# Kernel optimization log

Measured on AMD Instinct MI355X. Metric: run time of the kernel, lower is better.

Reference implementation:

```python
import jax, jax.numpy as jnp
import numpy as np

B, C, N, H = 8, 256, 1024, 8

def setup_inputs() -> dict:
    key = jax.random.key(0)
    ks = jax.random.split(key, 6)
    x = jax.random.normal(ks[0], (B, C, 3, N), jnp.float32)
    scale = 1.0 / np.sqrt(C).astype(np.float32)
    Wq = jax.random.normal(ks[1], (C, C), jnp.float32) * scale
    Wk = jax.random.normal(ks[2], (C, C), jnp.float32) * scale
    Wv = jax.random.normal(ks[3], (C, C), jnp.float32) * scale
    Wp = jax.random.normal(ks[4], (C, C), jnp.float32) * scale
    mask = jax.random.randint(ks[5], (B, N), 0, 2).astype(bool)  # True = padded
    return {"x": x, "Wq": Wq, "Wk": Wk, "Wv": Wv, "Wp": Wp, "mask": mask}

def _vn_linear(W, x):
    # VNLinear: channel-mixing linear (no bias) over the C axis of [B, C, 3, N]
    return jnp.einsum('oc,bcdn->bodn', W, x)

def _to_heads(t):
    # [B, C, 3, N] -> [B, H, N, (C//H)*3]
    hd = C // H
    return t.reshape(B, H, hd, 3, N).transpose(0, 1, 4, 2, 3).reshape(B, H, N, hd * 3)

def reference(x, Wq, Wk, Wv, Wp, mask):
    hd = C // H
    D = hd * 3
    q = _to_heads(_vn_linear(Wq, x))
    k = _to_heads(_vn_linear(Wk, x))
    v = _to_heads(_vn_linear(Wv, x))
    att = jnp.einsum('bhnd,bhmd->bhnm', q, k) * (1.0 / np.sqrt(D).astype(np.float32))
    att = jnp.where(mask[:, None, None, :], -jnp.inf, att)
    att = jax.nn.softmax(att, axis=-1)
    y = jnp.einsum('bhnm,bhmd->bhnd', att, v)
    # [B, H, N, D] -> [B, H, D, N] -> [B, H, hd, 3, N] -> [B, C, 3, N]
    y = y.transpose(0, 1, 3, 2).reshape(B, H, hd, 3, N).reshape(B, C, 3, N)
    return _vn_linear(Wp, y)
```

## Files before the change

kernel.cpp:

```cpp
#include <hip/hip_runtime.h>
#include <hip/hip_bf16.h>
#include <math.h>

#define B_ 8
#define C_ 256
#define N_ 1024
#define H_ 8
#define DH 96
#define BHN (C_*3*N_)
#define SC 0.10206207261596575f

typedef _Float16 half8 __attribute__((ext_vector_type(8)));
typedef float f32x4 __attribute__((ext_vector_type(4)));
typedef float f32x16 __attribute__((ext_vector_type(16)));

typedef __attribute__((address_space(1))) void gvoid;
typedef __attribute__((address_space(3))) void lvoid;
__device__ inline void gl_lds16(const _Float16* g, _Float16* l) {
  __builtin_amdgcn_global_load_lds((gvoid*)g, (lvoid*)l, 16, 0, 0);
}

typedef __fp16 fp16x2 __attribute__((ext_vector_type(2)));
union H2U { fp16x2 h2; unsigned u; };
__device__ inline unsigned pkh(float a, float b) {
  H2U x; x.h2 = __builtin_amdgcn_cvt_pkrtz(a, b); return x.u;
}
union PF { half8 v; unsigned u[4]; };

__device__ inline void plswap(unsigned& a, unsigned& b) {
  asm volatile("v_permlane32_swap_b32 %0, %1" : "+v"(a), "+v"(b));
}

__global__ void mask_bits_kernel(const unsigned* __restrict__ mraw,
                                 unsigned long long* __restrict__ mb) {
  __shared__ int notI, notF;
  if (threadIdx.x == 0) { notI = 0; notF = 0; }
  __syncthreads();
  int li = 0, lf = 0;
  for (int i = threadIdx.x; i < 2048; i += 256) {
    unsigned w = mraw[i];
    if (w > 1u) li = 1;
    if (w != 0u && w != 0x3F800000u) lf = 1;
  }
  if (li) atomicOr(&notI, 1);
  if (lf) atomicOr(&notF, 1);
  __syncthreads();
  const int tid = threadIdx.x;
  if (tid < 128) {
    int base = tid * 64;
    unsigned long long bits = 0;
    if (!notI) {
      for (int j = 0; j < 64; ++j)
        bits |= (unsigned long long)(mraw[base + j] & 1u) << j;
    } else if (!notF) {
      for (int j = 0; j < 64; ++j)
        bits |= (unsigned long long)(mraw[base + j] != 0u ? 1 : 0) << j;
    } else {
      const unsigned char* m8 = (const unsigned char*)mraw;
      for (int j = 0; j < 64; ++j)
        bits |= (unsigned long long)(m8[base + j] ? 1 : 0) << j;
    }
    mb[tid] = bits;
  }
}

__global__ void convw_kernel(const float* __restrict__ Wq,
                             const float* __restrict__ Wk,
                             const float* __restrict__ Wv,
                             const float* __restrict__ Wp,
                             _Float16* __restrict__ Wh) {
  int idx = blockIdx.x * 256 + threadIdx.x;
  int e0 = idx * 8;
  const float* src = (e0 < 65536) ? Wq
                   : (e0 < 131072) ? Wk
                   : (e0 < 196608) ? Wv : Wp;
  int off = e0 & 65535;
  float4 a = *(const float4*)&src[off];
  float4 b = *(const float4*)&src[off + 4];
  _Float16 t[8] = {(_Float16)a.x, (_Float16)a.y, (_Float16)a.z, (_Float16)a.w,
                   (_Float16)b.x, (_Float16)b.y, (_Float16)b.z, (_Float16)b.w};
  *(uint4*)&Wh[e0] = *(uint4*)t;
}

__global__ __launch_bounds__(256) void convxt_kernel(
    const float* __restrict__ x, _Float16* __restrict__ XT) {
  __shared__ _Float16 T[64][65];
  const int m0 = blockIdx.x * 64;
  const int c0 = blockIdx.y * 64;
  const int b = blockIdx.z;
  const float* xb = x + (size_t)b * BHN;
  _Float16* ob = XT + (size_t)b * BHN;
  const int t = threadIdx.x;
#pragma unroll
  for (int i = 0; i < 16; ++i) {
    int e = t + i * 256;
    int c = e >> 6, m = e & 63;
    T[m][c] = (_Float16)xb[(size_t)(c0 + c) * 3072 + m0 + m];
  }
  __syncthreads();
#pragma unroll
  for (int i = 0; i < 2; ++i) {
    int e = t + i * 256;
    int m = e >> 3, ch = e & 7;
    _Float16 tmp[8];
#pragma unroll
    for (int j = 0; j < 8; ++j) tmp[j] = T[m][ch * 8 + j];
    *(uint4*)&ob[(size_t)(m0 + m) * 256 + c0 + ch * 8] = *(uint4*)tmp;
  }
}

template <int MODE>
__global__ __launch_bounds__(256, 4) void mgemm_kernel(
    const _Float16* __restrict__ Wh, int woff,
    const _Float16* __restrict__ Xn,
    _Float16* __restrict__ O0, _Float16* __restrict__ O1,
    _Float16* __restrict__ O2, float* __restrict__ Of, int nw) {
  const int zz = blockIdx.z;
  const int w = zz % nw;
  const int b = zz / nw;
  const _Float16* Wb = Wh + (size_t)(woff + w) * 65536;
  const _Float16* Bb = Xn + (size_t)b * BHN;
  const int o0 = blockIdx.y * 128;
  const int bn0 = blockIdx.x * 128;

  __shared__ __align__(16) _Float16 Ah[4096];
  __shared__ __align__(16) _Float16 Bh[4096];

  const int tid = threadIdx.x;
  const int wave = tid >> 6;
  const int lane = tid & 63;
  const int lg = lane >> 4, ll = lane & 15;
  const int wm = wave >> 1, wn = wave & 1;
  const int r0 = tid >> 2, c4 = tid & 3;

  f32x4 acc[4][4];
#pragma unroll
  for (int mi = 0; mi < 4; ++mi)
#pragma unroll
    for (int ni = 0; ni < 4; ++ni) acc[mi][ni] = (f32x4){0.f, 0.f, 0.f, 0.f};

  for (int k0 = 0; k0 < 256; k0 += 32) {
    gl_lds16(Wb + (size_t)(o0 + r0) * 256 + k0 + c4 * 8, &Ah[wave * 512]);
    gl_lds16(Wb + (size_t)(o0 + 64 + r0) * 256 + k0 + c4 * 8,
             &Ah[2048 + wave * 512]);
    gl_lds16(Bb + (size_t)(bn0 + r0) * 256 + k0 + c4 * 8, &Bh[wave * 512]);
    gl_lds16(Bb + (size_t)(bn0 + 64 + r0) * 256 + k0 + c4 * 8,
             &Bh[2048 + wave * 512]);
    __syncthreads();
    half8 af[4], bf[4];
#pragma unroll
    for (int mi = 0; mi < 4; ++mi)
      af[mi] = *(const half8*)&Ah[(wm * 64 + mi * 16 + ll) * 32 + lg * 8];
#pragma unroll
    for (int ni = 0; ni < 4; ++ni)
      bf[ni] = *(const half8*)&Bh[(wn * 64 + ni * 16 + ll) * 32 + lg * 8];
#pragma unroll
    for (int mi = 0; mi < 4; ++mi)
#pragma unroll
      for (int ni = 0; ni < 4; ++ni)
        acc[mi][ni] = __builtin_amdgcn_mfma_f32_16x16x32_f16(
            af[mi], bf[ni], acc[mi][ni], 0, 0, 0);
    __syncthreads();
  }

#pragma unroll
  for (int mi = 0; mi < 4; ++mi) {
#pragma unroll
    for (int ni = 0; ni < 4; ++ni) {
      int o = o0 + wm * 64 + mi * 16 + lg * 4;
      int n = bn0 + wn * 64 + ni * 16 + ll;
      if constexpr (MODE == 1) {
        float* Ofb = Of + (size_t)b * BHN;
#pragma unroll
        for (int r = 0; r < 4; ++r)
          Ofb[(size_t)(o + r) * 3072 + n] = acc[mi][ni][r];
      } else {
        if (w == 2) {
          _Float16* Oc = O2 + (size_t)b * BHN;
#pragma unroll
          for (int r = 0; r < 4; ++r)
            Oc[(size_t)(o + r) * 3072 + n] = (_Float16)acc[mi][ni][r];
        } else {
          _Float16* On = ((w == 0) ? O0 : O1) + (size_t)b * BHN;
          float qs = (w == 0) ? SC : 1.0f;
          _Float16 t4[4];
#pragma unroll
          for (int r = 0; r < 4; ++r) t4[r] = (_Float16)(acc[mi][ni][r] * qs);
          *(uint2*)&On[(size_t)n * 256 + o] = *(uint2*)t4;
        }
      }
    }
  }
}

__global__ __launch_bounds__(256, 2) void attn_kernel(
    const _Float16* __restrict__ qh, const _Float16* __restrict__ kh,
    const _Float16* __restrict__ vh,
    const unsigned long long* __restrict__ mbits,
    _Float16* __restrict__ yT) {
  const int gid = blockIdx.x;
  const int bh = gid & 63;
  const int qt = gid >> 6;
  const int b = bh >> 3, h = bh & 7;
  const int n0 = qt * 128;

  __shared__ __align__(16) _Float16 Qs[12288];
  __shared__ __align__(16) _Float16 KsL[2][6144];
  __shared__ __align__(16) _Float16 VtL[2][6144];

  const int tid = threadIdx.x;
  const int lane = tid & 63;
  const int wave = tid >> 6;
  const int hi = lane >> 5;
  const int lq = lane & 31;
  const int wq0 = wave * 32;

  const _Float16* qb = qh + (size_t)b * BHN;
  const _Float16* kb = kh + (size_t)b * BHN;
  const _Float16* vb = vh + (size_t)b * BHN;

  const _Float16* ksrc[3];
  const _Float16* vsrc[3];
#pragma unroll
  for (int r = 0; r < 3; ++r) {
    int p = r * 4 + wave;
    ksrc[r] = kb + (size_t)((p >> 2) * 1024 + lane) * 256 + h * 32 + (p & 3) * 8;
    int G = (r * 4 + wave) * 64 + lane;
    int kp = G / 96, d = G - kp * 96;
    vsrc[r] = vb + (size_t)(h * 32 + (d & 31)) * 3072 + (d >> 5) * 1024 + kp * 8;
  }

  auto stage_kv = [&](int cur) {
    _Float16* Kd = &KsL[cur][0];
    _Float16* Vd = &VtL[cur][0];
#pragma unroll
    for (int r = 0; r < 3; ++r) {
      gl_lds16(ksrc[r], &Kd[(r * 4 + wave) * 512]);
      gl_lds16(vsrc[r], &Vd[(r * 4 + wave) * 512]);
      ksrc[r] += 64 * 256;
      vsrc[r] += 64;
    }
  };

#pragma unroll
  for (int r = 0; r < 6; ++r) {
    int pc = r * 4 + wave;
    int p = pc >> 1;
    int q = (pc & 1) * 64 + lane;
    gl_lds16(qb + (size_t)((p >> 2) * 1024 + n0 + q) * 256 + h * 32 + (p & 3) * 8,
             &Qs[(r * 4 + wave) * 512]);
  }
  stage_kv(0);
  __syncthreads();
  stage_kv(1);

  half8 qf[6];
#pragma unroll
  for (int ks = 0; ks < 6; ++ks)
    qf[ks] = *(const half8*)&Qs[(((2 * ks + hi) * 128) + wq0 + lq) * 8];

  float M = 0.f, Lh = 0.f;
  f32x16 yacc[3];
#pragma unroll
  for (int dt = 0; dt < 3; ++dt)
#pragma unroll
    for (int r = 0; r < 16; ++r) yacc[dt][r] = 0.f;

  auto compute_tile = [&](int t, int cur) {
    const _Float16* Ksb = &KsL[cur][0];
    const _Float16* Vtb = &VtL[cur][0];
    const unsigned long long m64 = mbits[b * 16 + t];

    f32x16 s[2];
#pragma unroll
    for (int r = 0; r < 16; ++r) { s[0][r] = 0.f; s[1][r] = 0.f; }
    __builtin_amdgcn_s_setprio(1);
#pragma unroll
    for (int ks = 0; ks < 6; ++ks) {
      half8 kf0 = *(const half8*)&Ksb[(((2 * ks + hi) * 64) + lq) * 8];
      half8 kf1 = *(const half8*)&Ksb[(((2 * ks + hi) * 64) + 32 + lq) * 8];
      s[0] = __builtin_amdgcn_mfma_f32_32x32x16_f16(kf0, qf[ks], s[0], 0, 0, 0);
      s[1] = __builtin_amdgcn_mfma_f32_32x32x16_f16(kf1, qf[ks], s[1], 0, 0, 0);
    }
    __builtin_amdgcn_s_setprio(0);

    float mx = -1e30f;
#pragma unroll
    for (int nt = 0; nt < 2; ++nt) {
      unsigned wm = (unsigned)(m64 >> (nt * 32 + 4 * hi));
#pragma unroll
      for (int r = 0; r < 16; ++r) {
        float sv = s[nt][r];
        sv = ((wm >> ((r & 3) + 8 * (r >> 2))) & 1u) ? -1e30f : sv;
        s[nt][r] = sv;
        mx = fmaxf(mx, sv);
      }
    }
    if (__any(mx > M + 8.f)) {
      float mx2 = fmaxf(mx, __shfl_xor(mx, 32));
      float newM = fmaxf(M, mx2);
      float corr = __expf(M - newM);
      M = newM;
      Lh *= corr;
#pragma unroll
      for (int dt = 0; dt < 3; ++dt)
#pragma unroll
        for (int r = 0; r < 16; ++r) yacc[dt][r] *= corr;
    }
    float psum = 0.f;
#pragma unroll
    for (int nt = 0; nt < 2; ++nt)
#pragma unroll
      for (int r = 0; r < 16; ++r) {
        float p = __expf(s[nt][r] - M);
        s[nt][r] = p;
        psum += p;
      }
    Lh += psum;

#pragma unroll
    for (int nt = 0; nt < 2; ++nt) {
#pragma unroll
      for (int hf = 0; hf < 2; ++hf) {
        const int bs = hf * 8;
        unsigned A0 = pkh(s[nt][bs + 0], s[nt][bs + 1]);
        unsigned A1 = pkh(s[nt][bs + 2], s[nt][bs + 3]);
        unsigned B0 = pkh(s[nt][bs + 4], s[nt][bs + 5]);
        unsigned B1 = pkh(s[nt][bs + 6], s[nt][bs + 7]);
        plswap(A0, B0);
        plswap(A1, B1);
        PF pf;
        pf.u[0] = A0;
        pf.u[1] = A1;
        pf.u[2] = B0;
        pf.u[3] = B1;
        const int kt = nt * 2 + hf;
        __builtin_amdgcn_s_setprio(1);
#pragma unroll
        for (int dt = 0; dt < 3; ++dt) {
          half8 vf = *(const half8*)&Vtb[(((kt * 2 + hi) * 96) + dt * 32 + lq) * 8];
          yacc[dt] = __builtin_amdgcn_mfma_f32_32x32x16_f16(vf, pf.v, yacc[dt],
                                                            0, 0, 0);
        }
        __builtin_amdgcn_s_setprio(0);
      }
    }
  };

  compute_tile(0, 0);
  for (int t = 1; t < 16; ++t) {
    __syncthreads();
    if (t + 1 < 16) stage_kv((t + 1) & 1);
    compute_tile(t, t & 1);
  }

  float L = Lh + __shfl_xor(Lh, 32);
  float inv = (L > 0.f) ? 1.f / L : 0.f;
  _Float16* Ys = &Qs[wave * 3072];
#pragma unroll
  for (int dt = 0; dt < 3; ++dt)
#pragma unroll
    for (int r = 0; r < 16; ++r) {
      int dperm = dt * 32 + (r & 3) + 8 * (r >> 2) + 4 * hi;
      Ys[lq * 96 + dperm] = (_Float16)(yacc[dt][r] * inv);
    }
  _Float16* yb = yT + (size_t)b * BHN;
#pragma unroll
  for (int j = 0; j < 6; ++j) {
    int c = j * 64 + lane;
    int q = c / 12, p = c - q * 12;
    uint4 val = *(const uint4*)&Ys[q * 96 + p * 8];
    int dd = p >> 2, pi = p & 3;
    *(uint4*)&yb[(size_t)((dd << 10) + n0 + wq0 + q) * 256 + h * 32 + pi * 8] =
        val;
  }
}

extern "C" void kernel_launch(void* const* d_in, const int* in_sizes, int n_in,
                              void* d_out, int out_size, void* d_ws,
                              size_t ws_size, hipStream_t stream) {
  const float* x = (const float*)d_in[0];
  const float* Wq = (const float*)d_in[1];
  const float* Wk = (const float*)d_in[2];
  const float* Wv = (const float*)d_in[3];
  const float* Wp = (const float*)d_in[4];
  const unsigned* mask = (const unsigned*)d_in[5];
  float* out = (float*)d_out;

  _Float16* Wh = (_Float16*)d_ws;
  _Float16* XT = Wh + 4 * 65536;
  _Float16* qh = XT + (size_t)B_ * BHN;
  _Float16* kh = qh + (size_t)B_ * BHN;
  _Float16* vh = kh + (size_t)B_ * BHN;
  _Float16* yT = vh + (size_t)B_ * BHN;
  unsigned long long* mb = (unsigned long long*)(yT + (size_t)B_ * BHN);

  mask_bits_kernel<<<1, 256, 0, stream>>>(mask, mb);
  convw_kernel<<<128, 256, 0, stream>>>(Wq, Wk, Wv, Wp, Wh);
  convxt_kernel<<<dim3(48, 4, B_), 256, 0, stream>>>(x, XT);

  dim3 g1(24, 2, B_ * 3);
  mgemm_kernel<0><<<g1, 256, 0, stream>>>(Wh, 0, XT, qh, kh, vh, nullptr, 3);

  attn_kernel<<<dim3(512), 256, 0, stream>>>(qh, kh, vh, mb, yT);

  dim3 g3(24, 2, B_);
  mgemm_kernel<1><<<g3, 256, 0, stream>>>(Wh, 3, yT, nullptr, nullptr, nullptr,
                                          out, 1);
}
```

Before: 101.6 us.

## Load attention operands directly from global memory and use exp2 softmax

Removes the LDS staging of Q, K and V in the attention kernel: each wave now loads its MFMA fragments straight from global memory into registers, which eliminates the double-buffered shared-memory pipeline and its per-tile barriers. The query scale folds in log2(e) so the softmax can use the hardware exp2 instruction, and the rescale threshold moves from 8 to 12 to match the log2 domain. The epilogue writes y directly from registers instead of going through an LDS transpose. In exchange, global loads are narrower and less coalesced, there is no explicit prefetch overlap, and register pressure rises because of the K and V fragment arrays.

```diff
diff --git a/kernel.cpp b/kernel.cpp
--- a/kernel.cpp
+++ b/kernel.cpp
@@ -9,6 +9,7 @@
 #define DH 96
 #define BHN (C_*3*N_)
 #define SC 0.10206207261596575f
+#define SCL2 0.14722193f
 
 typedef _Float16 half8 __attribute__((ext_vector_type(8)));
 typedef float f32x4 __attribute__((ext_vector_type(4)));
@@ -19,6 +20,8 @@
 __device__ inline void gl_lds16(const _Float16* g, _Float16* l) {
   __builtin_amdgcn_global_load_lds((gvoid*)g, (lvoid*)l, 16, 0, 0);
 }
+
+__device__ inline float ex2(float x) { return __builtin_amdgcn_exp2f(x); }
 
 typedef __fp16 fp16x2 __attribute__((ext_vector_type(2)));
 union H2U { fp16x2 h2; unsigned u; };
@@ -182,7 +185,7 @@
             Oc[(size_t)(o + r) * 3072 + n] = (_Float16)acc[mi][ni][r];
         } else {
           _Float16* On = ((w == 0) ? O0 : O1) + (size_t)b * BHN;
-          float qs = (w == 0) ? SC : 1.0f;
+          float qs = (w == 0) ? SCL2 : 1.0f;
           _Float16 t4[4];
 #pragma unroll
           for (int r = 0; r < 4; ++r) t4[r] = (_Float16)(acc[mi][ni][r] * qs);
@@ -204,10 +207,6 @@
   const int b = bh >> 3, h = bh & 7;
   const int n0 = qt * 128;
 
-  __shared__ __align__(16) _Float16 Qs[12288];
-  __shared__ __align__(16) _Float16 KsL[2][6144];
-  __shared__ __align__(16) _Float16 VtL[2][6144];
-
   const int tid = threadIdx.x;
   const int lane = tid & 63;
   const int wave = tid >> 6;
@@ -219,45 +218,16 @@
   const _Float16* kb = kh + (size_t)b * BHN;
   const _Float16* vb = vh + (size_t)b * BHN;
 
-  const _Float16* ksrc[3];
-  const _Float16* vsrc[3];
-#pragma unroll
-  for (int r = 0; r < 3; ++r) {
-    int p = r * 4 + wave;
-    ksrc[r] = kb + (size_t)((p >> 2) * 1024 + lane) * 256 + h * 32 + (p & 3) * 8;
-    int G = (r * 4 + wave) * 64 + lane;
-    int kp = G / 96, d = G - kp * 96;
-    vsrc[r] = vb + (size_t)(h * 32 + (d & 31)) * 3072 + (d >> 5) * 1024 + kp * 8;
-  }
-
-  auto stage_kv = [&](int cur) {
-    _Float16* Kd = &KsL[cur][0];
-    _Float16* Vd = &VtL[cur][0];
-#pragma unroll
-    for (int r = 0; r < 3; ++r) {
-      gl_lds16(ksrc[r], &Kd[(r * 4 + wave) * 512]);
-      gl_lds16(vsrc[r], &Vd[(r * 4 + wave) * 512]);
-      ksrc[r] += 64 * 256;
-      vsrc[r] += 64;
-    }
-  };
-
-#pragma unroll
-  for (int r = 0; r < 6; ++r) {
-    int pc = r * 4 + wave;
-    int p = pc >> 1;
-    int q = (pc & 1) * 64 + lane;
-    gl_lds16(qb + (size_t)((p >> 2) * 1024 + n0 + q) * 256 + h * 32 + (p & 3) * 8,
-             &Qs[(r * 4 + wave) * 512]);
-  }
-  stage_kv(0);
-  __syncthreads();
-  stage_kv(1);
-
   half8 qf[6];
 #pragma unroll
-  for (int ks = 0; ks < 6; ++ks)
-    qf[ks] = *(const half8*)&Qs[(((2 * ks + hi) * 128) + wq0 + lq) * 8];
+  for (int ks = 0; ks < 6; ++ks) {
+    int pp = 2 * ks + hi;
+    int dd = pp >> 2, i0 = (pp & 3) * 8;
+    qf[ks] = *(const half8*)(qb +
+        (size_t)(dd * 1024 + n0 + wq0 + lq) * 256 + h * 32 + i0);
+  }
+
+  const _Float16* vrow = vb + (size_t)(h * 32 + lq) * 3072;
 
   float M = 0.f, Lh = 0.f;
   f32x16 yacc[3];
@@ -266,9 +236,26 @@
 #pragma unroll
     for (int r = 0; r < 16; ++r) yacc[dt][r] = 0.f;
 
-  auto compute_tile = [&](int t, int cur) {
-    const _Float16* Ksb = &KsL[cur][0];
-    const _Float16* Vtb = &VtL[cur][0];
+  for (int t = 0; t < 16; ++t) {
+    const int m0 = t * 64;
+    half8 kf[6][2];
+#pragma unroll
+    for (int ks = 0; ks < 6; ++ks) {
+      int pp = 2 * ks + hi;
+      int dd = pp >> 2, i0 = (pp & 3) * 8;
+      const _Float16* base =
+          kb + (size_t)(dd * 1024 + m0 + lq) * 256 + h * 32 + i0;
+      kf[ks][0] = *(const half8*)base;
+      kf[ks][1] = *(const half8*)(base + 32 * 256);
+    }
+    half8 vf[4][3];
+#pragma unroll
+    for (int kt = 0; kt < 4; ++kt)
+#pragma unroll
+      for (int dt = 0; dt < 3; ++dt)
+        vf[kt][dt] =
+            *(const half8*)(vrow + dt * 1024 + m0 + (kt * 2 + hi) * 8);
+
     const unsigned long long m64 = mbits[b * 16 + t];
 
     f32x16 s[2];
@@ -277,10 +264,10 @@
     __builtin_amdgcn_s_setprio(1);
 #pragma unroll
     for (int ks = 0; ks < 6; ++ks) {
-      half8 kf0 = *(const half8*)&Ksb[(((2 * ks + hi) * 64) + lq) * 8];
-      half8 kf1 = *(const half8*)&Ksb[(((2 * ks + hi) * 64) + 32 + lq) * 8];
-      s[0] = __builtin_amdgcn_mfma_f32_32x32x16_f16(kf0, qf[ks], s[0], 0, 0, 0);
-      s[1] = __builtin_amdgcn_mfma_f32_32x32x16_f16(kf1, qf[ks], s[1], 0, 0, 0);
+      s[0] = __builtin_amdgcn_mfma_f32_32x32x16_f16(kf[ks][0], qf[ks], s[0],
+                                                    0, 0, 0);
+      s[1] = __builtin_amdgcn_mfma_f32_32x32x16_f16(kf[ks][1], qf[ks], s[1],
+                                                    0, 0, 0);
     }
     __builtin_amdgcn_s_setprio(0);
 
@@ -296,10 +283,10 @@
         mx = fmaxf(mx, sv);
       }
     }
-    if (__any(mx > M + 8.f)) {
+    if (__any(mx > M + 12.f)) {
       float mx2 = fmaxf(mx, __shfl_xor(mx, 32));
       float newM = fmaxf(M, mx2);
-      float corr = __expf(M - newM);
+      float corr = ex2(M - newM);
       M = newM;
       Lh *= corr;
 #pragma unroll
@@ -312,7 +299,7 @@
     for (int nt = 0; nt < 2; ++nt)
 #pragma unroll
       for (int r = 0; r < 16; ++r) {
-        float p = __expf(s[nt][r] - M);
+        float p = ex2(s[nt][r] - M);
         s[nt][r] = p;
         psum += p;
       }
@@ -337,42 +324,29 @@
         const int kt = nt * 2 + hf;
         __builtin_amdgcn_s_setprio(1);
 #pragma unroll
-        for (int dt = 0; dt < 3; ++dt) {
-          half8 vf = *(const half8*)&Vtb[(((kt * 2 + hi) * 96) + dt * 32 + lq) * 8];
-          yacc[dt] = __builtin_amdgcn_mfma_f32_32x32x16_f16(vf, pf.v, yacc[dt],
-                                                            0, 0, 0);
-        }
+        for (int dt = 0; dt < 3; ++dt)
+          yacc[dt] = __builtin_amdgcn_mfma_f32_32x32x16_f16(
+              vf[kt][dt], pf.v, yacc[dt], 0, 0, 0);
         __builtin_amdgcn_s_setprio(0);
       }
     }
-  };
-
-  compute_tile(0, 0);
-  for (int t = 1; t < 16; ++t) {
-    __syncthreads();
-    if (t + 1 < 16) stage_kv((t + 1) & 1);
-    compute_tile(t, t & 1);
   }
 
   float L = Lh + __shfl_xor(Lh, 32);
   float inv = (L > 0.f) ? 1.f / L : 0.f;
-  _Float16* Ys = &Qs[wave * 3072];
-#pragma unroll
-  for (int dt = 0; dt < 3; ++dt)
-#pragma unroll
-    for (int r = 0; r < 16; ++r) {
-      int dperm = dt * 32 + (r & 3) + 8 * (r >> 2) + 4 * hi;
-      Ys[lq * 96 + dperm] = (_Float16)(yacc[dt][r] * inv);
-    }
   _Float16* yb = yT + (size_t)b * BHN;
 #pragma unroll
-  for (int j = 0; j < 6; ++j) {
-    int c = j * 64 + lane;
-    int q = c / 12, p = c - q * 12;
-    uint4 val = *(const uint4*)&Ys[q * 96 + p * 8];
-    int dd = p >> 2, pi = p & 3;
-    *(uint4*)&yb[(size_t)((dd << 10) + n0 + wq0 + q) * 256 + h * 32 + pi * 8] =
-        val;
+  for (int dt = 0; dt < 3; ++dt) {
+    _Float16* rowp =
+        yb + (size_t)(dt * 1024 + n0 + wq0 + lq) * 256 + h * 32 + hi * 4;
+#pragma unroll
+    for (int g = 0; g < 4; ++g) {
+      _Float16 t4[4];
+#pragma unroll
+      for (int j = 0; j < 4; ++j)
+        t4[j] = (_Float16)(yacc[dt][g * 4 + j] * inv);
+      *(uint2*)(rowp + g * 8) = *(uint2*)t4;
+    }
   }
 }
 
```

Measured after the change: 143.0 us. 40.8% more time.
